# Optimization experiments

Hardware: AMD Instinct MI355X
Metric: run time of the kernel (lower is better)

Reference implementation:

```python
import jax, jax.numpy as jnp
import numpy as np

M, K, N = 32768, 2048, 2048  # tokens, in_features, out_features
QMIN, QMAX = -128, 127


def setup_inputs() -> dict:
    key = jax.random.key(0)
    ks = jax.random.split(key, 7)
    x = jax.random.normal(ks[0], (M, K), dtype=jnp.float32).astype(jnp.float16)
    int_weight = jax.random.randint(ks[1], (N, K), QMIN, QMAX + 1, dtype=jnp.int32).astype(jnp.int8)
    # calibrated-looking asymmetric activation quant params (fp16 buffers, [num_steps]=1)
    act_delta = (jax.random.uniform(ks[2], (1,), dtype=jnp.float32) * 0.02 + 0.005).astype(jnp.float16)
    act_zp = jnp.round(jax.random.normal(ks[3], (1,), dtype=jnp.float32) * 8.0).astype(jnp.float16)
    # per-output-channel weight scales; fuse precomputed dequant buffers consistently
    w_delta = jax.random.uniform(ks[4], (N,), dtype=jnp.float32) * 0.002 + 1e-4
    act_times_weight_delta = (act_delta.astype(jnp.float32) * w_delta)[None, :]  # [1, N]
    w_row_sum = jnp.sum(int_weight.astype(jnp.float32), axis=1)  # [N]
    zp_times_weight_channel_sum = (act_zp.astype(jnp.float32) * w_row_sum * act_times_weight_delta[0])[None, :]  # [1, N]
    bias = jax.random.normal(ks[5], (N,), dtype=jnp.float32) * 0.02
    return {
        "input": x,
        "act_delta": act_delta,
        "act_zp": act_zp,
        "zp_times_weight_channel_sum": zp_times_weight_channel_sum,
        "act_times_weight_delta": act_times_weight_delta,
        "bias": bias,
        "int_weight": int_weight,
    }


def reference(input, act_delta, act_zp, zp_times_weight_channel_sum,
              act_times_weight_delta, bias, int_weight):
    # current_step == num_steps - 1 == 0
    delta = act_delta[0].astype(jnp.float32)
    zp = act_zp[0].astype(jnp.float32)
    atwd = act_times_weight_delta[0]            # [N] = act_delta * weight_delta
    zp_sum = zp_times_weight_channel_sum[0]     # [N] = zp * rowsum(W_int) * atwd
    # asymmetric int8 activation quantization: q = clip(round(x/delta + zp))
    q = jnp.clip(jnp.round(input.astype(jnp.float32) / delta + zp), QMIN, QMAX).astype(jnp.int8)
    # int8 GEMM with int32 accumulation: [M,K] x [K,N]
    acc = jnp.matmul(q.astype(jnp.int32), int_weight.astype(jnp.int32).T)
    # fused dequant + zero-point correction + bias, cast to fp16
    out = acc.astype(jnp.float32) * atwd - zp_sum + bias
    return out.astype(jnp.float16)
```

## Files before the change

kernel.cpp:

```cpp
#include <hip/hip_runtime.h>
#include <hip/hip_fp16.h>
#include <stdint.h>

typedef int i32x4 __attribute__((ext_vector_type(4)));

#define BM 256
#define BN 256
#define BKB 128
#define SLOT 65536
#define THREADS 512

__device__ __forceinline__ void gload_lds16(const void* g, void* l) {
  __builtin_amdgcn_global_load_lds(
      (const __attribute__((address_space(1))) unsigned int*)g,
      (__attribute__((address_space(3))) unsigned int*)l, 16, 0, 0);
}

__global__ __launch_bounds__(256) void quant_x_kernel(
    const float* __restrict__ x, const float* __restrict__ deltap,
    const float* __restrict__ zpp, int8_t* __restrict__ q, int n16) {
  const float rdelta = 1.0f / deltap[0];
  const float zp = zpp[0];
  for (int i = blockIdx.x * blockDim.x + threadIdx.x; i < n16;
       i += gridDim.x * blockDim.x) {
    const float4* src = (const float4*)x + (size_t)i * 4;
    int packed[4];
#pragma unroll
    for (int g = 0; g < 4; ++g) {
      float4 v = src[g];
      float f0 = fminf(127.f, fmaxf(-128.f, rintf(fmaf(v.x, rdelta, zp))));
      float f1 = fminf(127.f, fmaxf(-128.f, rintf(fmaf(v.y, rdelta, zp))));
      float f2 = fminf(127.f, fmaxf(-128.f, rintf(fmaf(v.z, rdelta, zp))));
      float f3 = fminf(127.f, fmaxf(-128.f, rintf(fmaf(v.w, rdelta, zp))));
      int q0 = (int)f0 & 255, q1 = (int)f1 & 255, q2 = (int)f2 & 255, q3 = (int)f3 & 255;
      packed[g] = q0 | (q1 << 8) | (q2 << 16) | (q3 << 24);
    }
    ((int4*)q)[i] = make_int4(packed[0], packed[1], packed[2], packed[3]);
  }
}

__global__ __launch_bounds__(256) void pack_w_kernel(
    const int* __restrict__ w, int8_t* __restrict__ wp, int n16) {
  int i = blockIdx.x * blockDim.x + threadIdx.x;
  if (i >= n16) return;
  const int4* src = (const int4*)w + (size_t)i * 4;
  int packed[4];
#pragma unroll
  for (int g = 0; g < 4; ++g) {
    int4 v = src[g];
    packed[g] = (v.x & 255) | ((v.y & 255) << 8) | ((v.z & 255) << 16) | ((v.w & 255) << 24);
  }
  ((int4*)wp)[i] = make_int4(packed[0], packed[1], packed[2], packed[3]);
}

__global__ __launch_bounds__(THREADS, 2) void gemm_i8_kernel(
    const int8_t* __restrict__ Aq, const int8_t* __restrict__ Bw,
    const float* __restrict__ atwd, const float* __restrict__ zpws,
    const float* __restrict__ bias, float* __restrict__ out,
    int Mc, int Nc, int Kc) {
  __shared__ int8_t lds[2 * SLOT];

  const int nwg = gridDim.x;
  int bid = blockIdx.x;
  if ((nwg & 7) == 0) bid = (bid & 7) * (nwg >> 3) + (bid >> 3);
  const int nbn = Nc / BN;
  const int bm = bid / nbn;
  const int bn = bid % nbn;

  const int tid = threadIdx.x;
  const size_t K = (size_t)Kc;
  const int NT = Kc / BKB;

  const int srow = tid >> 3;
  const int cs = tid & 7;
  const int cl = cs ^ (srow & 7);
  const int8_t* gA = Aq + ((size_t)(bm * BM + srow)) * K + cl * 16;
  const int8_t* gB = Bw + ((size_t)(bn * BN + srow)) * K + cl * 16;
  const size_t row64 = (size_t)64 * K;
  int8_t* ldst = &lds[tid * 16];

  auto stage = [&](int t, int slot) {
    int8_t* l = ldst + slot * SLOT;
    const size_t koff = (size_t)t * BKB;
#pragma unroll
    for (int r = 0; r < 4; ++r)
      gload_lds16(gA + koff + r * row64, l + r * 8192);
#pragma unroll
    for (int r = 0; r < 4; ++r)
      gload_lds16(gB + koff + r * row64, l + 32768 + r * 8192);
  };

  const int lane = tid & 63;
  const int wave = tid >> 6;
  const int wr = wave >> 2;
  const int wc = wave & 3;
  const int fr = lane & 15;
  const int kc = lane >> 4;
  const int swz = fr & 7;
  const int aRow = wr * 128 + fr;
  const int bRow = wc * 64 + fr;

  i32x4 acc[8][4] = {};

  stage(0, 0);
  asm volatile("s_waitcnt vmcnt(0)" ::: "memory");
  __builtin_amdgcn_s_barrier();
  __builtin_amdgcn_sched_barrier(0);

  for (int t = 0; t < NT; ++t) {
    const int8_t* sA = &lds[(t & 1) * SLOT];
    const int8_t* sB = sA + 32768;

    i32x4 af[8][2], bf[4][2];
#pragma unroll
    for (int ks = 0; ks < 2; ++ks) {
      const int co = ((ks * 4 + kc) ^ swz) << 4;
#pragma unroll
      for (int j = 0; j < 4; ++j)
        bf[j][ks] = *(const i32x4*)&sB[(bRow + j * 16) * 128 + co];
#pragma unroll
      for (int i = 0; i < 8; ++i)
        af[i][ks] = *(const i32x4*)&sA[(aRow + ((i & 3) * 16) + ((i >> 2) * 64)) * 128 + co];
    }

    if (t + 1 < NT) stage(t + 1, (t + 1) & 1);

#pragma unroll
    for (int ks = 0; ks < 2; ++ks)
#pragma unroll
      for (int i = 0; i < 8; ++i)
#pragma unroll
        for (int j = 0; j < 4; ++j)
          acc[i][j] = __builtin_amdgcn_mfma_i32_16x16x64_i8(
              af[((i >> 2) * 4) + (i & 3)][ks], bf[j][ks], acc[i][j], 0, 0, 0);

    if (t < NT - 1) {
      asm volatile("s_waitcnt vmcnt(0)" ::: "memory");
      __builtin_amdgcn_s_barrier();
      __builtin_amdgcn_sched_barrier(0);
    }
  }

  const int r4 = (lane >> 4) << 2;
  const int cn0 = bn * BN + wc * 64 + fr;
  float aw4[4], zs4[4], bs4[4];
#pragma unroll
  for (int j = 0; j < 4; ++j) {
    aw4[j] = atwd[cn0 + j * 16];
    zs4[j] = zpws[cn0 + j * 16];
    bs4[j] = bias[cn0 + j * 16];
  }
#pragma unroll
  for (int i = 0; i < 8; ++i) {
    const int mrow = ((i & 3) * 16) + ((i >> 2) * 64);
#pragma unroll
    for (int r = 0; r < 4; ++r) {
      const size_t rbase = (size_t)(bm * BM + wr * 128 + mrow + r4 + r) * (size_t)Nc;
#pragma unroll
      for (int j = 0; j < 4; ++j) {
        float v = (float)acc[i][j][r] * aw4[j] - zs4[j] + bs4[j];
        v = __half2float(__float2half(v));
        out[rbase + cn0 + j * 16] = v;
      }
    }
  }
}

extern "C" void kernel_launch(void* const* d_in, const int* in_sizes, int n_in,
                              void* d_out, int out_size, void* d_ws, size_t ws_size,
                              hipStream_t stream) {
  const float* x         = (const float*)d_in[0];
  const float* act_delta = (const float*)d_in[1];
  const float* act_zp    = (const float*)d_in[2];
  const float* zpws      = (const float*)d_in[3];
  const float* atwd      = (const float*)d_in[4];
  const float* bias      = (const float*)d_in[5];
  const int*   w32       = (const int*)d_in[6];
  float* out = (float*)d_out;

  const int N = in_sizes[5];
  const int K = in_sizes[6] / N;
  const int M = in_sizes[0] / K;

  int8_t* q  = (int8_t*)d_ws;
  int8_t* wp = q + (size_t)M * K;

  {
    int n16 = (M * K) / 16;
    int grid = (n16 + 255) / 256;
    if (grid > 2048) grid = 2048;
    quant_x_kernel<<<grid, 256, 0, stream>>>(x, act_delta, act_zp, q, n16);
  }
  {
    int n16 = (N * K) / 16;
    pack_w_kernel<<<(n16 + 255) / 256, 256, 0, stream>>>(w32, wp, n16);
  }
  {
    dim3 grid((M / BM) * (N / BN));
    gemm_i8_kernel<<<grid, THREADS, 0, stream>>>(q, wp, atwd, zpws, bias, out, M, N, K);
  }
}
```

Before: 245.8 us.

## Shrink M tile to 128 and use triple-buffered LDS with register double-buffering

Halves the block M tile to 128 rows and moves from double to triple LDS buffering. Global-to-LDS loads now run two stages ahead, with partial vmcnt waits instead of full drains. Fragments for the next k-step are read into a second register set while the current MFMAs run, to overlap LDS reads, global loads and math. The smaller tile halves per-wave accumulators and doubles the grid, but each block reuses B across fewer rows, so more global B traffic is needed per output.

```diff
diff --git a/kernel.cpp b/kernel.cpp
--- a/kernel.cpp
+++ b/kernel.cpp
@@ -4,10 +4,11 @@
 
 typedef int i32x4 __attribute__((ext_vector_type(4)));
 
-#define BM 256
+#define BM 128
 #define BN 256
 #define BKB 128
-#define SLOT 65536
+#define NSLOT 3
+#define SLOT_BYTES 49152
 #define THREADS 512
 
 __device__ __forceinline__ void gload_lds16(const void* g, void* l) {
@@ -58,7 +59,7 @@
     const float* __restrict__ atwd, const float* __restrict__ zpws,
     const float* __restrict__ bias, float* __restrict__ out,
     int Mc, int Nc, int Kc) {
-  __shared__ int8_t lds[2 * SLOT];
+  __shared__ int8_t lds[NSLOT * SLOT_BYTES];
 
   const int nwg = gridDim.x;
   int bid = blockIdx.x;
@@ -80,14 +81,14 @@
   int8_t* ldst = &lds[tid * 16];
 
   auto stage = [&](int t, int slot) {
-    int8_t* l = ldst + slot * SLOT;
+    int8_t* l = ldst + slot * SLOT_BYTES;
     const size_t koff = (size_t)t * BKB;
 #pragma unroll
+    for (int r = 0; r < 2; ++r)
+      gload_lds16(gA + koff + r * row64, l + r * 8192);
+#pragma unroll
     for (int r = 0; r < 4; ++r)
-      gload_lds16(gA + koff + r * row64, l + r * 8192);
-#pragma unroll
-    for (int r = 0; r < 4; ++r)
-      gload_lds16(gB + koff + r * row64, l + 32768 + r * 8192);
+      gload_lds16(gB + koff + r * row64, l + 16384 + r * 8192);
   };
 
   const int lane = tid & 63;
@@ -97,49 +98,58 @@
   const int fr = lane & 15;
   const int kc = lane >> 4;
   const int swz = fr & 7;
-  const int aRow = wr * 128 + fr;
+  const int aRow = wr * 64 + fr;
   const int bRow = wc * 64 + fr;
 
-  i32x4 acc[8][4] = {};
+  i32x4 acc[4][4] = {};
+  i32x4 fa0[4][2], fb0[4][2], fa1[4][2], fb1[4][2];
+
+#define READF(AF, BF, t)                                                      \
+  {                                                                           \
+    const int8_t* sA_ = &lds[((t) % NSLOT) * SLOT_BYTES];                     \
+    const int8_t* sB_ = sA_ + 16384;                                          \
+    _Pragma("unroll") for (int ks_ = 0; ks_ < 2; ++ks_) {                     \
+      const int co_ = ((ks_ * 4 + kc) ^ swz) << 4;                            \
+      _Pragma("unroll") for (int i_ = 0; i_ < 4; ++i_)                        \
+        AF[i_][ks_] = *(const i32x4*)&sA_[(aRow + i_ * 16) * 128 + co_];      \
+      _Pragma("unroll") for (int j_ = 0; j_ < 4; ++j_)                        \
+        BF[j_][ks_] = *(const i32x4*)&sB_[(bRow + j_ * 16) * 128 + co_];      \
+    }                                                                         \
+  }
+
+#define DOMFMA(AF, BF)                                                        \
+  _Pragma("unroll") for (int ks_ = 0; ks_ < 2; ++ks_)                         \
+    _Pragma("unroll") for (int i_ = 0; i_ < 4; ++i_)                          \
+      _Pragma("unroll") for (int j_ = 0; j_ < 4; ++j_)                        \
+        acc[i_][j_] = __builtin_amdgcn_mfma_i32_16x16x64_i8(                  \
+            AF[i_][ks_], BF[j_][ks_], acc[i_][j_], 0, 0, 0);
+
+#define SYNCN(N)                                                              \
+  asm volatile("s_waitcnt vmcnt(" #N ")" ::: "memory");                       \
+  asm volatile("s_waitcnt lgkmcnt(0)" ::: "memory");                          \
+  __builtin_amdgcn_s_barrier();                                               \
+  __builtin_amdgcn_sched_barrier(0);
 
   stage(0, 0);
-  asm volatile("s_waitcnt vmcnt(0)" ::: "memory");
-  __builtin_amdgcn_s_barrier();
-  __builtin_amdgcn_sched_barrier(0);
-
-  for (int t = 0; t < NT; ++t) {
-    const int8_t* sA = &lds[(t & 1) * SLOT];
-    const int8_t* sB = sA + 32768;
-
-    i32x4 af[8][2], bf[4][2];
-#pragma unroll
-    for (int ks = 0; ks < 2; ++ks) {
-      const int co = ((ks * 4 + kc) ^ swz) << 4;
-#pragma unroll
-      for (int j = 0; j < 4; ++j)
-        bf[j][ks] = *(const i32x4*)&sB[(bRow + j * 16) * 128 + co];
-#pragma unroll
-      for (int i = 0; i < 8; ++i)
-        af[i][ks] = *(const i32x4*)&sA[(aRow + ((i & 3) * 16) + ((i >> 2) * 64)) * 128 + co];
-    }
-
-    if (t + 1 < NT) stage(t + 1, (t + 1) & 1);
-
-#pragma unroll
-    for (int ks = 0; ks < 2; ++ks)
-#pragma unroll
-      for (int i = 0; i < 8; ++i)
-#pragma unroll
-        for (int j = 0; j < 4; ++j)
-          acc[i][j] = __builtin_amdgcn_mfma_i32_16x16x64_i8(
-              af[((i >> 2) * 4) + (i & 3)][ks], bf[j][ks], acc[i][j], 0, 0, 0);
-
-    if (t < NT - 1) {
-      asm volatile("s_waitcnt vmcnt(0)" ::: "memory");
-      __builtin_amdgcn_s_barrier();
-      __builtin_amdgcn_sched_barrier(0);
-    }
-  }
+  stage(1, 1);
+  SYNCN(6);
+  READF(fa0, fb0, 0);
+
+  for (int t = 0; t < NT; t += 2) {
+    if (t + 2 < NT) stage(t + 2, (t + 2) % NSLOT);
+    if (t + 2 < NT) { SYNCN(6); } else { SYNCN(0); }
+    if (t + 1 < NT) READF(fa1, fb1, t + 1);
+    DOMFMA(fa0, fb0);
+
+    if (t + 3 < NT) stage(t + 3, (t + 3) % NSLOT);
+    if (t + 3 < NT)      { SYNCN(6); }
+    else if (t + 2 < NT) { SYNCN(0); }
+    if (t + 2 < NT) READF(fa0, fb0, t + 2);
+    if (t + 1 < NT) DOMFMA(fa1, fb1);
+  }
+#undef READF
+#undef DOMFMA
+#undef SYNCN
 
   const int r4 = (lane >> 4) << 2;
   const int cn0 = bn * BN + wc * 64 + fr;
@@ -151,14 +161,13 @@
     bs4[j] = bias[cn0 + j * 16];
   }
 #pragma unroll
-  for (int i = 0; i < 8; ++i) {
-    const int mrow = ((i & 3) * 16) + ((i >> 2) * 64);
+  for (int mi = 0; mi < 4; ++mi) {
 #pragma unroll
     for (int r = 0; r < 4; ++r) {
-      const size_t rbase = (size_t)(bm * BM + wr * 128 + mrow + r4 + r) * (size_t)Nc;
+      const size_t rbase = (size_t)(bm * BM + wr * 64 + mi * 16 + r4 + r) * (size_t)Nc;
 #pragma unroll
       for (int j = 0; j < 4; ++j) {
-        float v = (float)acc[i][j][r] * aw4[j] - zs4[j] + bs4[j];
+        float v = (float)acc[mi][j][r] * aw4[j] - zs4[j] + bs4[j];
         v = __half2float(__float2half(v));
         out[rbase + cn0 + j * 16] = v;
       }
```

Result: slower. 256.5 us (+4.4%).

## Load B fragments directly from global into registers, halving LDS footprint

Applied to the files above, without the earlier changes.

The weight tile is no longer staged through LDS. Each wave loads its B fragments straight from global memory into registers, double-buffered across two register sets with the K loop unrolled by two. LDS then holds only the A tile (64KB instead of 128KB), which could allow more resident workgroups and cuts LDS traffic for B. In exchange, each of the two waves sharing a column slab re-reads the same B data from global/L2, register pressure goes up, and the loop assumes an even tile count.

```diff
diff --git a/kernel.cpp b/kernel.cpp
--- a/kernel.cpp
+++ b/kernel.cpp
@@ -7,7 +7,7 @@
 #define BM 256
 #define BN 256
 #define BKB 128
-#define SLOT 65536
+#define ASLOT 32768
 #define THREADS 512
 
 __device__ __forceinline__ void gload_lds16(const void* g, void* l) {
@@ -58,7 +58,7 @@
     const float* __restrict__ atwd, const float* __restrict__ zpws,
     const float* __restrict__ bias, float* __restrict__ out,
     int Mc, int Nc, int Kc) {
-  __shared__ int8_t lds[2 * SLOT];
+  __shared__ int8_t lds[2 * ASLOT];
 
   const int nwg = gridDim.x;
   int bid = blockIdx.x;
@@ -75,19 +75,15 @@
   const int cs = tid & 7;
   const int cl = cs ^ (srow & 7);
   const int8_t* gA = Aq + ((size_t)(bm * BM + srow)) * K + cl * 16;
-  const int8_t* gB = Bw + ((size_t)(bn * BN + srow)) * K + cl * 16;
   const size_t row64 = (size_t)64 * K;
   int8_t* ldst = &lds[tid * 16];
 
-  auto stage = [&](int t, int slot) {
-    int8_t* l = ldst + slot * SLOT;
+  auto stageA = [&](int t, int slot) {
+    int8_t* l = ldst + slot * ASLOT;
     const size_t koff = (size_t)t * BKB;
 #pragma unroll
     for (int r = 0; r < 4; ++r)
       gload_lds16(gA + koff + r * row64, l + r * 8192);
-#pragma unroll
-    for (int r = 0; r < 4; ++r)
-      gload_lds16(gB + koff + r * row64, l + 32768 + r * 8192);
   };
 
   const int lane = tid & 63;
@@ -98,48 +94,52 @@
   const int kc = lane >> 4;
   const int swz = fr & 7;
   const int aRow = wr * 128 + fr;
-  const int bRow = wc * 64 + fr;
+
+  const int8_t* gB = Bw + ((size_t)(bn * BN + wc * 64 + fr)) * K + kc * 16;
 
   i32x4 acc[8][4] = {};
-
-  stage(0, 0);
+  i32x4 bfA[4][2], bfB[4][2];
+
+#define LOADB(REG, t)                                                         \
+  _Pragma("unroll") for (int j_ = 0; j_ < 4; ++j_)                            \
+    _Pragma("unroll") for (int ks_ = 0; ks_ < 2; ++ks_)                       \
+      REG[j_][ks_] = *(const i32x4*)&gB[(size_t)(j_ * 16) * K +               \
+                                        (size_t)(t) * BKB + ks_ * 64];
+
+#define TILE(t, CUR, NXT)                                                     \
+  {                                                                           \
+    const int8_t* sA_ = &lds[((t) & 1) * ASLOT];                              \
+    if ((t) + 1 < NT) { LOADB(NXT, (t) + 1); stageA((t) + 1, ((t) + 1) & 1); }\
+    _Pragma("unroll") for (int ks_ = 0; ks_ < 2; ++ks_) {                     \
+      const int co_ = ((ks_ * 4 + kc) ^ swz) << 4;                            \
+      i32x4 af_[8];                                                           \
+      _Pragma("unroll") for (int i_ = 0; i_ < 8; ++i_)                        \
+        af_[i_] = *(const i32x4*)&sA_[(aRow + ((i_ & 3) * 16) +               \
+                                      ((i_ >> 2) * 64)) * 128 + co_];         \
+      _Pragma("unroll") for (int i_ = 0; i_ < 8; ++i_)                        \
+        _Pragma("unroll") for (int j_ = 0; j_ < 4; ++j_)                      \
+          acc[i_][j_] = __builtin_amdgcn_mfma_i32_16x16x64_i8(                \
+              af_[i_], CUR[j_][ks_], acc[i_][j_], 0, 0, 0);                   \
+    }                                                                         \
+    if ((t) < NT - 1) {                                                       \
+      asm volatile("s_waitcnt vmcnt(0)" ::: "memory");                        \
+      __builtin_amdgcn_s_barrier();                                           \
+      __builtin_amdgcn_sched_barrier(0);                                      \
+    }                                                                         \
+  }
+
+  stageA(0, 0);
+  LOADB(bfA, 0);
   asm volatile("s_waitcnt vmcnt(0)" ::: "memory");
   __builtin_amdgcn_s_barrier();
   __builtin_amdgcn_sched_barrier(0);
 
-  for (int t = 0; t < NT; ++t) {
-    const int8_t* sA = &lds[(t & 1) * SLOT];
-    const int8_t* sB = sA + 32768;
-
-    i32x4 af[8][2], bf[4][2];
-#pragma unroll
-    for (int ks = 0; ks < 2; ++ks) {
-      const int co = ((ks * 4 + kc) ^ swz) << 4;
-#pragma unroll
-      for (int j = 0; j < 4; ++j)
-        bf[j][ks] = *(const i32x4*)&sB[(bRow + j * 16) * 128 + co];
-#pragma unroll
-      for (int i = 0; i < 8; ++i)
-        af[i][ks] = *(const i32x4*)&sA[(aRow + ((i & 3) * 16) + ((i >> 2) * 64)) * 128 + co];
-    }
-
-    if (t + 1 < NT) stage(t + 1, (t + 1) & 1);
-
-#pragma unroll
-    for (int ks = 0; ks < 2; ++ks)
-#pragma unroll
-      for (int i = 0; i < 8; ++i)
-#pragma unroll
-        for (int j = 0; j < 4; ++j)
-          acc[i][j] = __builtin_amdgcn_mfma_i32_16x16x64_i8(
-              af[((i >> 2) * 4) + (i & 3)][ks], bf[j][ks], acc[i][j], 0, 0, 0);
-
-    if (t < NT - 1) {
-      asm volatile("s_waitcnt vmcnt(0)" ::: "memory");
-      __builtin_amdgcn_s_barrier();
-      __builtin_amdgcn_sched_barrier(0);
-    }
-  }
+  for (int t = 0; t < NT; t += 2) {
+    TILE(t, bfA, bfB);
+    TILE(t + 1, bfB, bfA);
+  }
+#undef TILE
+#undef LOADB
 
   const int r4 = (lane >> 4) << 2;
   const int cn0 = bn * BN + wc * 64 + fr;
```

Result: slower. 496.6 us (+102.1%).
